# Performance work log

Hardware: AMD Instinct MI355X
Metric: run time of the kernel (lower is better)

Reference implementation:

```python
import jax, jax.numpy as jnp
import numpy as np

D = 4096
H = 4 * D
EPS = 1e-5


def layer_norm(x, g, b):
    mu = jnp.mean(x, axis=-1, keepdims=True)
    var = jnp.mean(jnp.square(x - mu), axis=-1, keepdims=True)
    return (x - mu) * jax.lax.rsqrt(var + EPS) * g + b


def setup_inputs() -> dict:
    key = jax.random.key(0)
    ks = jax.random.split(key, 8)
    s = 0.02
    return {
        "x": jax.random.normal(ks[0], (2, 2048, D), dtype=jnp.float32),
        "Wq": jax.random.normal(ks[1], (D, D), dtype=jnp.float32) * s,
        "bq": jnp.zeros((D,), jnp.float32),
        "Wk": jax.random.normal(ks[2], (D, D), dtype=jnp.float32) * s,
        "bk": jnp.zeros((D,), jnp.float32),
        "Wv": jax.random.normal(ks[3], (D, D), dtype=jnp.float32) * s,
        "bv": jnp.zeros((D,), jnp.float32),
        "Wo": jax.random.normal(ks[4], (D, D), dtype=jnp.float32) * s,
        "bo": jnp.zeros((D,), jnp.float32),
        "g1": jnp.ones((D,), jnp.float32),
        "b1": jnp.zeros((D,), jnp.float32),
        "g2": jnp.ones((D,), jnp.float32),
        "b2": jnp.zeros((D,), jnp.float32),
        "W1": jax.random.normal(ks[5], (D, H), dtype=jnp.float32) * s,
        "bi1": jnp.zeros((H,), jnp.float32),
        "W2": jax.random.normal(ks[6], (H, D), dtype=jnp.float32) * s,
        "bi2": jnp.zeros((D,), jnp.float32),
    }


def reference(x, Wq, bq, Wk, bk, Wv, bv, Wo, bo, g1, b1, g2, b2, W1, bi1, W2, bi2):
    # single-head attention, scale = sqrt(D) (as in the source)
    Q = x @ Wq + bq          # [B, S, D]
    K = x @ Wk + bk
    V = x @ Wv + bv
    scores = jnp.einsum("bsd,btd->bst", Q, K) / jnp.sqrt(jnp.float32(D))
    attn = jax.nn.softmax(scores, axis=-1) @ V   # [B, S, D]
    x = attn @ Wo + bo + x
    x = layer_norm(x, g1, b1)
    h = jax.nn.gelu(x @ W1 + bi1, approximate=False)  # torch nn.GELU default = exact erf
    x = h @ W2 + bi2 + x
    x = layer_norm(x, g2, b2)
    return x
```

## Files before the change

### kernel.cpp

```cpp
#include <hip/hip_runtime.h>
#include <hip/hip_bf16.h>

typedef __bf16 bf16x8 __attribute__((ext_vector_type(8)));
typedef float  f32x4  __attribute__((ext_vector_type(4)));
typedef unsigned short u16;
typedef unsigned int   u32;

#define DEV __device__ __forceinline__

DEV u16 f2bu(float f){ union{float f; u32 i;} x; x.f=f; u32 r=x.i+0x7FFFu+((x.i>>16)&1u); return (u16)(r>>16); }
DEV u32 pack2(float a, float b){ return (u32)f2bu(a) | ((u32)f2bu(b)<<16); }

DEV void gload16(const u16* g, u16* l){
  __builtin_amdgcn_global_load_lds((const __attribute__((address_space(1))) void*)g,
                                   (__attribute__((address_space(3))) void*)l, 16, 0, 0);
}

template<int BIAS, int GELU, int RESF32, int OUTF32>
DEV void gemm_body(
    const u16* __restrict__ A, const u16* __restrict__ Bt,
    const float* __restrict__ bias, const float* __restrict__ resid,
    float* __restrict__ outF, u16* __restrict__ outB,
    int M, int N, int K, int SWZ,
    long long sA, long long sB, long long sC)
{
  __shared__ __align__(16) u16 As[4][8192];
  __shared__ __align__(16) u16 Bs[4][8192];

  const int tid  = threadIdx.x;
  const int lane = tid & 63;
  const int wave = tid >> 6;
  const int wm = wave >> 2;
  const int wn = wave & 3;

  int bx = blockIdx.x, by = blockIdx.y;
  if (SWZ) {
    const int gx = gridDim.x, gy = gridDim.y;
    const int f  = by * gx + bx;
    const int S  = gy << 4;
    const int s  = f / S;
    const int r  = f - s * S;
    bx = (s << 4) + (r & 15);
    by = r >> 4;
  }
  const int rowBase = by * 256;
  const int colBase = bx * 256;

  const u16* Ag = A + (size_t)blockIdx.z * sA + (size_t)rowBase * K;
  const u16* Bg = Bt + (size_t)blockIdx.z * sB + (size_t)colBase * K;

  const int qsw = (lane & 3) ^ ((lane >> 3) & 3);
  const u16* apA0 = Ag + (size_t)(wave*32 + (lane>>2)) * K + qsw*8;
  const u16* apA1 = apA0 + (size_t)16 * K;
  const u16* apB0 = Bg + (size_t)(wave*32 + (lane>>2)) * K + qsw*8;
  const u16* apB1 = apB0 + (size_t)16 * K;
  u16* dA0 = &As[0][wave*1024 + lane*8];
  u16* dA1 = dA0 + 512;
  u16* dB0 = &Bs[0][wave*1024 + lane*8];
  u16* dB1 = dB0 + 512;

#define STAGE(t) { const int _b = (t) & 3; const size_t _k = (size_t)(t) * 32;          \
    gload16(apA0 + _k, dA0 + _b*8192); gload16(apA1 + _k, dA1 + _b*8192);               \
    gload16(apB0 + _k, dB0 + _b*8192); gload16(apB1 + _k, dB1 + _b*8192); }

  const int r15 = lane & 15;
  const int gp  = (lane >> 4) ^ ((lane >> 1) & 3);
  const u16* rdA = &As[0][(wm*128 + r15)*32 + gp*8];
  const u16* rdB = &Bs[0][(wn*64  + r15)*32 + gp*8];

  f32x4 acc[8][4];
  const f32x4 fz = {0.f,0.f,0.f,0.f};
#pragma unroll
  for (int m=0;m<8;++m)
#pragma unroll
    for (int n=0;n<4;++n) acc[m][n] = fz;

  const int KT = K >> 5;
  STAGE(0);
  if (KT > 1) STAGE(1);
  if (KT > 2) STAGE(2);

  for (int t = 0; t < KT; ++t) {
    const int rem = KT - t;
    if (rem > 2)      asm volatile("s_waitcnt vmcnt(8)" ::: "memory");
    else if (rem > 1) asm volatile("s_waitcnt vmcnt(4)" ::: "memory");
    else              asm volatile("s_waitcnt vmcnt(0)" ::: "memory");
    __builtin_amdgcn_s_barrier();
    asm volatile("" ::: "memory");

    const u16* pa = rdA + (t & 3) * 8192;
    const u16* pb = rdB + (t & 3) * 8192;
    bf16x8 a[8], b[4];
#pragma unroll
    for (int m=0;m<8;++m) a[m] = *(const bf16x8*)(pa + m*512);
#pragma unroll
    for (int n=0;n<4;++n) b[n] = *(const bf16x8*)(pb + n*512);

    if (t + 3 < KT) STAGE(t + 3);

    __builtin_amdgcn_s_setprio(1);
#pragma unroll
    for (int m=0;m<8;++m)
#pragma unroll
      for (int n=0;n<4;++n)
        acc[m][n] = __builtin_amdgcn_mfma_f32_16x16x32_bf16(a[m], b[n], acc[m][n], 0,0,0);
    __builtin_amdgcn_s_setprio(0);
  }
#undef STAGE

  const long long cb = (long long)blockIdx.z * sC;
  const int q4 = (lane >> 4) * 4;
#pragma unroll
  for (int m=0;m<8;++m){
    const int row0 = rowBase + wm*128 + m*16 + q4;
#pragma unroll
    for (int n=0;n<4;++n){
      const int col = colBase + wn*64 + n*16 + r15;
      float bb = 0.f;
      if (BIAS) bb = bias[col];
#pragma unroll
      for (int r=0;r<4;++r){
        float v = acc[m][n][r] + bb;
        if (GELU) v = 0.5f*v*(1.f+erff(v*0.70710678118654752f));
        const size_t oi = (size_t)cb + (size_t)(row0+r)*N + col;
        if (RESF32) v += resid[oi];
        if (OUTF32) outF[oi] = v;
        else        outB[oi] = f2bu(v);
      }
    }
  }
}

template<int OUTF32>
DEV void gemm128_body(
    const u16* __restrict__ A, const u16* __restrict__ Bt,
    float* __restrict__ outF, u16* __restrict__ outB,
    int M, int N, int K,
    long long sA, long long sB, long long sC)
{
  __shared__ __align__(16) u16 As[4][4096];
  __shared__ __align__(16) u16 Bs[4][8192];

  const int tid  = threadIdx.x;
  const int lane = tid & 63;
  const int wave = tid >> 6;
  const int wm = wave >> 2;
  const int wn = wave & 3;

  const int rowBase = blockIdx.y * 128;
  const int colBase = blockIdx.x * 256;

  const u16* Ag = A + (size_t)blockIdx.z * sA + (size_t)rowBase * K;
  const u16* Bg = Bt + (size_t)blockIdx.z * sB + (size_t)colBase * K;

  const int qsw = (lane & 3) ^ ((lane >> 3) & 3);
  const u16* apA0 = Ag + (size_t)(wave*16 + (lane>>2)) * K + qsw*8;
  const u16* apB0 = Bg + (size_t)(wave*32 + (lane>>2)) * K + qsw*8;
  const u16* apB1 = apB0 + (size_t)16 * K;
  u16* dA0 = &As[0][wave*512  + lane*8];
  u16* dB0 = &Bs[0][wave*1024 + lane*8];
  u16* dB1 = dB0 + 512;

#define STAGE1(t) { const int _b = (t) & 3; const size_t _k = (size_t)(t) * 32;         \
    gload16(apA0 + _k, dA0 + _b*4096);                                                  \
    gload16(apB0 + _k, dB0 + _b*8192); gload16(apB1 + _k, dB1 + _b*8192); }

  const int r15 = lane & 15;
  const int gp  = (lane >> 4) ^ ((lane >> 1) & 3);
  const u16* rdA = &As[0][(wm*64 + r15)*32 + gp*8];
  const u16* rdB = &Bs[0][(wn*64 + r15)*32 + gp*8];

  f32x4 acc[4][4];
  const f32x4 fz = {0.f,0.f,0.f,0.f};
#pragma unroll
  for (int m=0;m<4;++m)
#pragma unroll
    for (int n=0;n<4;++n) acc[m][n] = fz;

  const int KT = K >> 5;
  STAGE1(0);
  if (KT > 1) STAGE1(1);
  if (KT > 2) STAGE1(2);

  for (int t = 0; t < KT; ++t) {
    const int rem = KT - t;
    if (rem > 2)      asm volatile("s_waitcnt vmcnt(6)" ::: "memory");
    else if (rem > 1) asm volatile("s_waitcnt vmcnt(3)" ::: "memory");
    else              asm volatile("s_waitcnt vmcnt(0)" ::: "memory");
    __builtin_amdgcn_s_barrier();
    asm volatile("" ::: "memory");

    const u16* pa = rdA + (t & 3) * 4096;
    const u16* pb = rdB + (t & 3) * 8192;
    bf16x8 a[4], b[4];
#pragma unroll
    for (int m=0;m<4;++m) a[m] = *(const bf16x8*)(pa + m*512);
#pragma unroll
    for (int n=0;n<4;++n) b[n] = *(const bf16x8*)(pb + n*512);

    if (t + 3 < KT) STAGE1(t + 3);

    __builtin_amdgcn_s_setprio(1);
#pragma unroll
    for (int m=0;m<4;++m)
#pragma unroll
      for (int n=0;n<4;++n)
        acc[m][n] = __builtin_amdgcn_mfma_f32_16x16x32_bf16(a[m], b[n], acc[m][n], 0,0,0);
    __builtin_amdgcn_s_setprio(0);
  }
#undef STAGE1

  const long long cb = (long long)blockIdx.z * sC;
  const int q4 = (lane >> 4) * 4;
#pragma unroll
  for (int m=0;m<4;++m){
    const int row0 = rowBase + wm*64 + m*16 + q4;
#pragma unroll
    for (int n=0;n<4;++n){
      const int col = colBase + wn*64 + n*16 + r15;
#pragma unroll
      for (int r=0;r<4;++r){
        const float v = acc[m][n][r];
        const size_t oi = (size_t)cb + (size_t)(row0+r)*N + col;
        if (OUTF32) outF[oi] = v;
        else        outB[oi] = f2bu(v);
      }
    }
  }
}

#define GEMM_KERNEL(NAME, BIAS, GELU, RESF32, OUTF32)                      \
__global__ __launch_bounds__(512, 2) void NAME(                           \
    const u16* __restrict__ A, const u16* __restrict__ Bt,                 \
    const float* __restrict__ bias, const float* __restrict__ resid,       \
    float* __restrict__ outF, u16* __restrict__ outB,                      \
    int M, int N, int K, int SWZ,                                          \
    long long sA, long long sB, long long sC) {                            \
  gemm_body<BIAS,GELU,RESF32,OUTF32>(A,Bt,bias,resid,outF,outB,M,N,K,SWZ,sA,sB,sC); }

GEMM_KERNEL(gemm_q,   1,0,0,0)
GEMM_KERNEL(gemm_k,   1,0,0,0)
GEMM_KERNEL(gemm_v,   1,0,0,0)
GEMM_KERNEL(gemm_pv,  0,0,0,0)
GEMM_KERNEL(gemm_o,   1,0,1,1)
GEMM_KERNEL(gemm_f1,  1,1,0,0)
GEMM_KERNEL(gemm_f2,  1,0,1,1)

__global__ __launch_bounds__(512, 2) void gemm_qkt(
    const u16* __restrict__ A, const u16* __restrict__ Bt,
    float* __restrict__ outF, u16* __restrict__ outB,
    int M, int N, int K,
    long long sA, long long sB, long long sC) {
  gemm128_body<1>(A, Bt, outF, outB, M, N, K, sA, sB, sC);
}

__global__ __launch_bounds__(256) void tr_f32_bf16(
    const float* __restrict__ in, u16* __restrict__ out, int R, int C)
{
  __shared__ float tile[64][65];
  const int t = threadIdx.x;
  const int tr = blockIdx.y*64, tc = blockIdx.x*64;
  const int c4 = (t&15)*4;
#pragma unroll
  for (int i=0;i<4;++i){
    const int r = i*16 + (t>>4);
    const float4 v = *reinterpret_cast<const float4*>(&in[(size_t)(tr+r)*C + tc + c4]);
    tile[r][c4+0]=v.x; tile[r][c4+1]=v.y; tile[r][c4+2]=v.z; tile[r][c4+3]=v.w;
  }
  __syncthreads();
#pragma unroll
  for (int i=0;i<4;++i){
    const int c = i*16 + (t>>4);
    uint2 o;
    o.x = pack2(tile[c4+0][c], tile[c4+1][c]);
    o.y = pack2(tile[c4+2][c], tile[c4+3][c]);
    *reinterpret_cast<uint2*>(&out[(size_t)(tc+c)*R + tr + c4]) = o;
  }
}

__global__ __launch_bounds__(256) void tr_bf16(
    const u16* __restrict__ in, u16* __restrict__ out, int R, int C,
    long long sIn, long long sOut)
{
  __shared__ u16 tile[64][72];
  const long long z = blockIdx.z;
  in  += z*sIn; out += z*sOut;
  const int t = threadIdx.x;
  const int tr = blockIdx.y*64, tc = blockIdx.x*64;
  const int c4 = (t&15)*4;
#pragma unroll
  for (int i=0;i<4;++i){
    const int r = i*16 + (t>>4);
    const uint2 v = *reinterpret_cast<const uint2*>(&in[(size_t)(tr+r)*C + tc + c4]);
    tile[r][c4+0]=(u16)(v.x&0xffffu); tile[r][c4+1]=(u16)(v.x>>16);
    tile[r][c4+2]=(u16)(v.y&0xffffu); tile[r][c4+3]=(u16)(v.y>>16);
  }
  __syncthreads();
#pragma unroll
  for (int i=0;i<4;++i){
    const int c = i*16 + (t>>4);
    uint2 o;
    o.x = (u32)tile[c4+0][c] | ((u32)tile[c4+1][c]<<16);
    o.y = (u32)tile[c4+2][c] | ((u32)tile[c4+3][c]<<16);
    *reinterpret_cast<uint2*>(&out[(size_t)(tc+c)*R + tr + c4]) = o;
  }
}

__global__ __launch_bounds__(256) void cvt_f32_bf16(
    const float* __restrict__ in, u16* __restrict__ out, int n4)
{
  const int i = blockIdx.x*256 + threadIdx.x;
  if (i >= n4) return;
  const float4 v = reinterpret_cast<const float4*>(in)[i];
  uint2 o; o.x = pack2(v.x,v.y); o.y = pack2(v.z,v.w);
  reinterpret_cast<uint2*>(out)[i] = o;
}

__global__ __launch_bounds__(256) void softmax2048(
    const float* __restrict__ S, u16* __restrict__ P, float scale)
{
  const size_t row = blockIdx.x;
  const float4* src = reinterpret_cast<const float4*>(S + row*2048);
  const int t = threadIdx.x, lane = t&63, wave = t>>6;
  const float4 a = src[t], b = src[t+256];
  float v[8] = {a.x,a.y,a.z,a.w,b.x,b.y,b.z,b.w};
  float m = -3.4e38f;
#pragma unroll
  for (int i=0;i<8;++i){ v[i]*=scale; m = fmaxf(m, v[i]); }
#pragma unroll
  for (int o=32;o>0;o>>=1) m = fmaxf(m, __shfl_xor(m, o));
  __shared__ float red[8];
  if (lane==0) red[wave]=m;
  __syncthreads();
  m = fmaxf(fmaxf(red[0],red[1]), fmaxf(red[2],red[3]));
  float s = 0.f;
#pragma unroll
  for (int i=0;i<8;++i){ v[i] = __expf(v[i]-m); s += v[i]; }
#pragma unroll
  for (int o=32;o>0;o>>=1) s += __shfl_xor(s, o);
  if (lane==0) red[4+wave]=s;
  __syncthreads();
  s = red[4]+red[5]+red[6]+red[7];
  const float r = 1.f/s;
  uint2 o1, o2;
  o1.x = pack2(v[0]*r, v[1]*r); o1.y = pack2(v[2]*r, v[3]*r);
  o2.x = pack2(v[4]*r, v[5]*r); o2.y = pack2(v[6]*r, v[7]*r);
  uint2* dst = reinterpret_cast<uint2*>(P + row*2048);
  dst[t] = o1; dst[t+256] = o2;
}

template<int WB>
__global__ __launch_bounds__(256) void layernorm4096(
    const float* __restrict__ X, const float* __restrict__ g,
    const float* __restrict__ b, float* __restrict__ Yf, u16* __restrict__ Yb)
{
  const size_t row = blockIdx.x;
  const float4* src = reinterpret_cast<const float4*>(X + row*4096);
  const int t = threadIdx.x, lane = t&63, wave = t>>6;
  float4 xv[4];
  float sum=0.f, ss=0.f;
#pragma unroll
  for (int i=0;i<4;++i){
    xv[i] = src[t + 256*i];
    sum += xv[i].x+xv[i].y+xv[i].z+xv[i].w;
    ss  += xv[i].x*xv[i].x + xv[i].y*xv[i].y + xv[i].z*xv[i].z + xv[i].w*xv[i].w;
  }
#pragma unroll
  for (int o=32;o>0;o>>=1){ sum += __shfl_xor(sum,o); ss += __shfl_xor(ss,o); }
  __shared__ float rs[4], rq[4];
  if (lane==0){ rs[wave]=sum; rq[wave]=ss; }
  __syncthreads();
  sum = rs[0]+rs[1]+rs[2]+rs[3];
  ss  = rq[0]+rq[1]+rq[2]+rq[3];
  const float mean = sum * (1.f/4096.f);
  const float var  = ss * (1.f/4096.f) - mean*mean;
  const float rstd = rsqrtf(var + 1e-5f);
#pragma unroll
  for (int i=0;i<4;++i){
    const int i4 = t + 256*i;
    const float4 gv = reinterpret_cast<const float4*>(g)[i4];
    const float4 bvv = reinterpret_cast<const float4*>(b)[i4];
    float4 y;
    y.x = (xv[i].x-mean)*rstd*gv.x + bvv.x;
    y.y = (xv[i].y-mean)*rstd*gv.y + bvv.y;
    y.z = (xv[i].z-mean)*rstd*gv.z + bvv.z;
    y.w = (xv[i].w-mean)*rstd*gv.w + bvv.w;
    reinterpret_cast<float4*>(Yf + row*4096)[i4] = y;
    if (WB){
      uint2 o; o.x = pack2(y.x,y.y); o.y = pack2(y.z,y.w);
      reinterpret_cast<uint2*>(Yb + row*4096)[i4] = o;
    }
  }
}

extern "C" void kernel_launch(void* const* d_in, const int* in_sizes, int n_in,
                              void* d_out, int out_size, void* d_ws, size_t ws_size,
                              hipStream_t stream)
{
  constexpr int D = 4096, HD = 16384, S = 2048, B = 2;
  constexpr int NT = B*S;
  const float* x   = (const float*)d_in[0];
  const float* Wq  = (const float*)d_in[1];
  const float* bq  = (const float*)d_in[2];
  const float* Wk  = (const float*)d_in[3];
  const float* bk  = (const float*)d_in[4];
  const float* Wv  = (const float*)d_in[5];
  const float* bvp = (const float*)d_in[6];
  const float* Wo  = (const float*)d_in[7];
  const float* bo  = (const float*)d_in[8];
  const float* g1  = (const float*)d_in[9];
  const float* b1  = (const float*)d_in[10];
  const float* g2  = (const float*)d_in[11];
  const float* b2  = (const float*)d_in[12];
  const float* W1  = (const float*)d_in[13];
  const float* bi1 = (const float*)d_in[14];
  const float* W2  = (const float*)d_in[15];
  const float* bi2 = (const float*)d_in[16];

  char* ws = (char*)d_ws;
  const size_t MB32 = 33554432;
  u16* WqT = (u16*)(ws + 0*MB32);
  u16* WkT = (u16*)(ws + 1*MB32);
  u16* WvT = (u16*)(ws + 2*MB32);
  u16* WoT = (u16*)(ws + 3*MB32);
  u16* W1T = (u16*)(ws + 0*MB32);
  u16* xb  = (u16*)(ws + 4*MB32);
  u16* Qb  = (u16*)(ws + 5*MB32);
  u16* Kb  = (u16*)(ws + 6*MB32);
  u16* Vb  = (u16*)(ws + 7*MB32);
  u16* W2T = (u16*)(ws + 4*MB32);
  u16* Vt  = (u16*)(ws + 8*MB32);
  float* scoresF = (float*)(ws + 9*MB32);
  u16* Pb  = (u16*)(ws + 10*MB32);
  u16* Ab  = (u16*)(ws + 10*MB32 + 16777216);
  u16* hB  = (u16*)(ws + 8*MB32);
  float* x1raw = (float*)(ws + 12*MB32);
  float* x2raw = (float*)(ws + 12*MB32);
  float* x1f   = (float*)(ws + 14*MB32);
  u16*   x1b   = (u16*)(ws + 16*MB32);

  const dim3 blk(256), blkG(512);
  const long long SD = (long long)S*D, SS = (long long)S*S, DS = (long long)D*S;

  tr_f32_bf16<<<dim3(D/64, D/64), blk, 0, stream>>>(Wq, WqT, D, D);
  tr_f32_bf16<<<dim3(D/64, D/64), blk, 0, stream>>>(Wk, WkT, D, D);
  tr_f32_bf16<<<dim3(D/64, D/64), blk, 0, stream>>>(Wv, WvT, D, D);
  tr_f32_bf16<<<dim3(D/64, D/64), blk, 0, stream>>>(Wo, WoT, D, D);
  cvt_f32_bf16<<<dim3((NT*D/4)/256), blk, 0, stream>>>(x, xb, NT*D/4);

  gemm_q<<<dim3(D/256, NT/256, 1), blkG, 0, stream>>>(xb, WqT, bq,  nullptr, nullptr, Qb, NT, D, D, 1, 0,0,0);
  gemm_k<<<dim3(D/256, NT/256, 1), blkG, 0, stream>>>(xb, WkT, bk,  nullptr, nullptr, Kb, NT, D, D, 1, 0,0,0);
  gemm_v<<<dim3(D/256, NT/256, 1), blkG, 0, stream>>>(xb, WvT, bvp, nullptr, nullptr, Vb, NT, D, D, 1, 0,0,0);
  tr_bf16<<<dim3(D/64, S/64, B), blk, 0, stream>>>(Vb, Vt, S, D, SD, SD);

  gemm_qkt<<<dim3(S/256, S/128, B), blkG, 0, stream>>>(Qb, Kb, scoresF, nullptr, S, S, D, SD, SD, SS);
  softmax2048<<<dim3(B*S), blk, 0, stream>>>(scoresF, Pb, 0.015625f);
  gemm_pv<<<dim3(D/256, S/256, B), blkG, 0, stream>>>(Pb, Vt, nullptr, nullptr, nullptr, Ab, S, D, S, 0, SS, DS, SD);

  gemm_o<<<dim3(D/256, NT/256, 1), blkG, 0, stream>>>(Ab, WoT, bo, x, x1raw, nullptr, NT, D, D, 1, 0,0,0);
  layernorm4096<1><<<dim3(NT), blk, 0, stream>>>(x1raw, g1, b1, x1f, x1b);

  tr_f32_bf16<<<dim3(HD/64, D/64), blk, 0, stream>>>(W1, W1T, D, HD);
  gemm_f1<<<dim3(HD/256, NT/256, 1), blkG, 0, stream>>>(x1b, W1T, bi1, nullptr, nullptr, hB, NT, HD, D, 1, 0,0,0);
  tr_f32_bf16<<<dim3(D/64, HD/64), blk, 0, stream>>>(W2, W2T, HD, D);
  gemm_f2<<<dim3(D/256, NT/256, 1), blkG, 0, stream>>>(hB, W2T, bi2, x1f, x2raw, nullptr, NT, D, HD, 1, 0,0,0);
  layernorm4096<0><<<dim3(NT), blk, 0, stream>>>(x2raw, g2, b2, (float*)d_out, nullptr);
}
```

Measured before the change: 2.183 ms.

## Add 8-wave ping-pong GEMM with K=64 tiles for the two FFN GEMMs

Adds a new GEMM body that uses K=64 tiles with a 2-stage LDS double buffer and an XOR-swizzled layout. Each iteration is split into four MFMA quadrants, and global-to-LDS staging and LDS fragment reads are interleaved between barriers. The two FFN GEMMs, which dominate the FLOPs, are switched to it, while the attention GEMMs stay on the old 4-stage K=32 kernel. It trades a deeper prefetch pipeline for finer-grained overlap, at the cost of many more barriers per iteration.

```diff
diff --git a/kernel.cpp b/kernel.cpp
--- a/kernel.cpp
+++ b/kernel.cpp
@@ -15,6 +15,10 @@
   __builtin_amdgcn_global_load_lds((const __attribute__((address_space(1))) void*)g,
                                    (__attribute__((address_space(3))) void*)l, 16, 0, 0);
 }
+
+#define FENCE asm volatile("" ::: "memory")
+#define BAR   __builtin_amdgcn_s_barrier()
+#define LGKM0 asm volatile("s_waitcnt lgkmcnt(0)" ::: "memory")
 
 template<int BIAS, int GELU, int RESF32, int OUTF32>
 DEV void gemm_body(
@@ -26,12 +30,10 @@
 {
   __shared__ __align__(16) u16 As[4][8192];
   __shared__ __align__(16) u16 Bs[4][8192];
-
   const int tid  = threadIdx.x;
   const int lane = tid & 63;
   const int wave = tid >> 6;
-  const int wm = wave >> 2;
-  const int wn = wave & 3;
+  const int wm = wave >> 2, wn = wave & 3;
 
   int bx = blockIdx.x, by = blockIdx.y;
   if (SWZ) {
@@ -85,8 +87,7 @@
     if (rem > 2)      asm volatile("s_waitcnt vmcnt(8)" ::: "memory");
     else if (rem > 1) asm volatile("s_waitcnt vmcnt(4)" ::: "memory");
     else              asm volatile("s_waitcnt vmcnt(0)" ::: "memory");
-    __builtin_amdgcn_s_barrier();
-    asm volatile("" ::: "memory");
+    BAR; FENCE;
 
     const u16* pa = rdA + (t & 3) * 8192;
     const u16* pb = rdB + (t & 3) * 8192;
@@ -131,6 +132,180 @@
   }
 }
 
+template<int BIAS, int GELU, int RESF32, int OUTF32>
+DEV void gemm8_body(
+    const u16* __restrict__ A, const u16* __restrict__ Bt,
+    const float* __restrict__ bias, const float* __restrict__ resid,
+    float* __restrict__ outF, u16* __restrict__ outB,
+    int M, int N, int K, int SWZ,
+    long long sA, long long sB, long long sC)
+{
+  __shared__ __align__(16) u16 As[2][2][8192];
+  __shared__ __align__(16) u16 Bs[2][2][8192];
+
+  const int tid  = threadIdx.x;
+  const int lane = tid & 63;
+  const int wave = tid >> 6;
+  const int wm = wave >> 2;
+  const int wn = wave & 3;
+
+  int bx = blockIdx.x, by = blockIdx.y;
+  if (SWZ) {
+    const int gx = gridDim.x, gy = gridDim.y;
+    const int f  = by * gx + bx;
+    const int S  = gy << 4;
+    const int s  = f / S;
+    const int r  = f - s * S;
+    bx = (s << 4) + (r & 15);
+    by = r >> 4;
+  }
+  const int rowBase = by * 256;
+  const int colBase = bx * 256;
+
+  const u16* Ag = A + (size_t)blockIdx.z * sA + (size_t)rowBase * K;
+  const u16* Bg = Bt + (size_t)blockIdx.z * sB + (size_t)colBase * K;
+
+  const int swzk = ((tid & 7) ^ ((tid >> 3) & 7)) * 8;
+  const u16* gAh[2], *gBh[2];
+  gAh[0] = Ag + (size_t)(tid>>3) * K + swzk;
+  gAh[1] = Ag + (size_t)(128 + (tid>>3)) * K + swzk;
+  gBh[0] = Bg + (size_t)(tid>>3) * K + swzk;
+  gBh[1] = Bg + (size_t)(128 + (tid>>3)) * K + swzk;
+  const size_t rstep = (size_t)64 * K;
+  u16* dAb = &As[0][0][0] + tid*8;
+  u16* dBb = &Bs[0][0][0] + tid*8;
+
+#define STG_A(h, tt) { u16* _d = dAb + (((tt)&1)<<14) + ((h)<<13);                      \
+    const u16* _g = gAh[h] + (size_t)(tt)*64;                                           \
+    gload16(_g, _d); gload16(_g + rstep, _d + 4096); }
+#define STG_B(h, tt) { u16* _d = dBb + (((tt)&1)<<14) + ((h)<<13);                      \
+    const u16* _g = gBh[h] + (size_t)(tt)*64;                                           \
+    gload16(_g, _d); gload16(_g + rstep, _d + 4096); }
+
+  const int r15 = lane & 15;
+  const int c4 = lane >> 4, e = lane & 7;
+  const int ch0 = (c4 ^ e) * 8;
+  const int ch1 = ((4 + c4) ^ e) * 8;
+  const u16* rA0 = &As[0][wm][0] + r15*64 + ch0;
+  const u16* rA1 = &As[0][wm][0] + r15*64 + ch1;
+  const u16* rB0 = &Bs[0][wn>>1][0] + ((wn&1)*64 + r15)*64 + ch0;
+  const u16* rB1 = &Bs[0][wn>>1][0] + ((wn&1)*64 + r15)*64 + ch1;
+
+  f32x4 acc[8][4];
+  const f32x4 fz = {0.f,0.f,0.f,0.f};
+#pragma unroll
+  for (int m=0;m<8;++m)
+#pragma unroll
+    for (int n=0;n<4;++n) acc[m][n] = fz;
+
+  const int KT = K >> 6;
+  STG_A(0,0); STG_A(1,0); STG_B(0,0); STG_B(1,0);
+  if (KT > 1) {
+    STG_A(0,1); STG_B(0,1); STG_B(1,1);
+    asm volatile("s_waitcnt vmcnt(6)" ::: "memory");
+  } else {
+    asm volatile("s_waitcnt vmcnt(0)" ::: "memory");
+  }
+  BAR; FENCE;
+
+  for (int t = 0; t < KT; ++t) {
+    const int dsel = (t & 1) << 14;
+    const bool s1 = (t + 1 < KT), s2 = (t + 2 < KT);
+    const u16* pa0 = rA0 + dsel; const u16* pa1 = rA1 + dsel;
+    const u16* pb0 = rB0 + dsel; const u16* pb1 = rB1 + dsel;
+    bf16x8 a[4][2], b0[2][2], b1[2][2];
+
+#pragma unroll
+    for (int i=0;i<4;++i){ a[i][0] = *(const bf16x8*)(pa0 + i*1024);
+                           a[i][1] = *(const bf16x8*)(pa1 + i*1024); }
+#pragma unroll
+    for (int n=0;n<2;++n){ b0[n][0] = *(const bf16x8*)(pb0 + n*1024);
+                           b0[n][1] = *(const bf16x8*)(pb1 + n*1024); }
+    if (s1) STG_A(1, t+1);
+    FENCE; BAR; LGKM0;
+    __builtin_amdgcn_s_setprio(1);
+#pragma unroll
+    for (int m=0;m<4;++m)
+#pragma unroll
+      for (int n=0;n<2;++n){
+        acc[m][n] = __builtin_amdgcn_mfma_f32_16x16x32_bf16(a[m][0], b0[n][0], acc[m][n], 0,0,0);
+        acc[m][n] = __builtin_amdgcn_mfma_f32_16x16x32_bf16(a[m][1], b0[n][1], acc[m][n], 0,0,0);
+      }
+    __builtin_amdgcn_s_setprio(0);
+    FENCE; BAR;
+
+#pragma unroll
+    for (int n=0;n<2;++n){ b1[n][0] = *(const bf16x8*)(pb0 + (2+n)*1024);
+                           b1[n][1] = *(const bf16x8*)(pb1 + (2+n)*1024); }
+    FENCE; BAR; LGKM0;
+    __builtin_amdgcn_s_setprio(1);
+#pragma unroll
+    for (int m=0;m<4;++m)
+#pragma unroll
+      for (int n=0;n<2;++n){
+        acc[m][2+n] = __builtin_amdgcn_mfma_f32_16x16x32_bf16(a[m][0], b1[n][0], acc[m][2+n], 0,0,0);
+        acc[m][2+n] = __builtin_amdgcn_mfma_f32_16x16x32_bf16(a[m][1], b1[n][1], acc[m][2+n], 0,0,0);
+      }
+    __builtin_amdgcn_s_setprio(0);
+    FENCE; BAR;
+
+#pragma unroll
+    for (int i=0;i<4;++i){ a[i][0] = *(const bf16x8*)(pa0 + (4+i)*1024);
+                           a[i][1] = *(const bf16x8*)(pa1 + (4+i)*1024); }
+    if (s2) STG_B(0, t+2);
+    FENCE; BAR; LGKM0;
+    __builtin_amdgcn_s_setprio(1);
+#pragma unroll
+    for (int m=0;m<4;++m)
+#pragma unroll
+      for (int n=0;n<2;++n){
+        acc[4+m][2+n] = __builtin_amdgcn_mfma_f32_16x16x32_bf16(a[m][0], b1[n][0], acc[4+m][2+n], 0,0,0);
+        acc[4+m][2+n] = __builtin_amdgcn_mfma_f32_16x16x32_bf16(a[m][1], b1[n][1], acc[4+m][2+n], 0,0,0);
+      }
+    __builtin_amdgcn_s_setprio(0);
+    FENCE; BAR;
+
+    if (s2) { STG_A(0, t+2); STG_B(1, t+2);
+              asm volatile("s_waitcnt vmcnt(6)" ::: "memory"); }
+    else    { asm volatile("s_waitcnt vmcnt(0)" ::: "memory"); }
+    FENCE; BAR;
+    __builtin_amdgcn_s_setprio(1);
+#pragma unroll
+    for (int m=0;m<4;++m)
+#pragma unroll
+      for (int n=0;n<2;++n){
+        acc[4+m][n] = __builtin_amdgcn_mfma_f32_16x16x32_bf16(a[m][0], b0[n][0], acc[4+m][n], 0,0,0);
+        acc[4+m][n] = __builtin_amdgcn_mfma_f32_16x16x32_bf16(a[m][1], b0[n][1], acc[4+m][n], 0,0,0);
+      }
+    __builtin_amdgcn_s_setprio(0);
+    FENCE; BAR;
+  }
+#undef STG_A
+#undef STG_B
+
+  const long long cb = (long long)blockIdx.z * sC;
+  const int q4 = (lane >> 4) * 4;
+#pragma unroll
+  for (int m=0;m<8;++m){
+    const int row0 = rowBase + wm*128 + m*16 + q4;
+#pragma unroll
+    for (int n=0;n<4;++n){
+      const int col = colBase + wn*64 + n*16 + r15;
+      float bb = 0.f;
+      if (BIAS) bb = bias[col];
+#pragma unroll
+      for (int r=0;r<4;++r){
+        float v = acc[m][n][r] + bb;
+        if (GELU) v = 0.5f*v*(1.f+erff(v*0.70710678118654752f));
+        const size_t oi = (size_t)cb + (size_t)(row0+r)*N + col;
+        if (RESF32) v += resid[oi];
+        if (OUTF32) outF[oi] = v;
+        else        outB[oi] = f2bu(v);
+      }
+    }
+  }
+}
+
 template<int OUTF32>
 DEV void gemm128_body(
     const u16* __restrict__ A, const u16* __restrict__ Bt,
@@ -140,12 +315,10 @@
 {
   __shared__ __align__(16) u16 As[4][4096];
   __shared__ __align__(16) u16 Bs[4][8192];
-
   const int tid  = threadIdx.x;
   const int lane = tid & 63;
   const int wave = tid >> 6;
-  const int wm = wave >> 2;
-  const int wn = wave & 3;
+  const int wm = wave >> 2, wn = wave & 3;
 
   const int rowBase = blockIdx.y * 128;
   const int colBase = blockIdx.x * 256;
@@ -187,8 +360,7 @@
     if (rem > 2)      asm volatile("s_waitcnt vmcnt(6)" ::: "memory");
     else if (rem > 1) asm volatile("s_waitcnt vmcnt(3)" ::: "memory");
     else              asm volatile("s_waitcnt vmcnt(0)" ::: "memory");
-    __builtin_amdgcn_s_barrier();
-    asm volatile("" ::: "memory");
+    BAR; FENCE;
 
     const u16* pa = rdA + (t & 3) * 4096;
     const u16* pb = rdB + (t & 3) * 8192;
@@ -229,22 +401,22 @@
   }
 }
 
-#define GEMM_KERNEL(NAME, BIAS, GELU, RESF32, OUTF32)                      \
+#define GEMM_KERNEL(NAME, BODY, BIAS, GELU, RESF32, OUTF32)                \
 __global__ __launch_bounds__(512, 2) void NAME(                           \
     const u16* __restrict__ A, const u16* __restrict__ Bt,                 \
     const float* __restrict__ bias, const float* __restrict__ resid,       \
     float* __restrict__ outF, u16* __restrict__ outB,                      \
     int M, int N, int K, int SWZ,                                          \
     long long sA, long long sB, long long sC) {                            \
-  gemm_body<BIAS,GELU,RESF32,OUTF32>(A,Bt,bias,resid,outF,outB,M,N,K,SWZ,sA,sB,sC); }
-
-GEMM_KERNEL(gemm_q,   1,0,0,0)
-GEMM_KERNEL(gemm_k,   1,0,0,0)
-GEMM_KERNEL(gemm_v,   1,0,0,0)
-GEMM_KERNEL(gemm_pv,  0,0,0,0)
-GEMM_KERNEL(gemm_o,   1,0,1,1)
-GEMM_KERNEL(gemm_f1,  1,1,0,0)
-GEMM_KERNEL(gemm_f2,  1,0,1,1)
+  BODY<BIAS,GELU,RESF32,OUTF32>(A,Bt,bias,resid,outF,outB,M,N,K,SWZ,sA,sB,sC); }
+
+GEMM_KERNEL(gemm_q,   gemm_body,  1,0,0,0)
+GEMM_KERNEL(gemm_k,   gemm_body,  1,0,0,0)
+GEMM_KERNEL(gemm_v,   gemm_body,  1,0,0,0)
+GEMM_KERNEL(gemm_pv,  gemm_body,  0,0,0,0)
+GEMM_KERNEL(gemm_o,   gemm_body,  1,0,1,1)
+GEMM_KERNEL(gemm8_f1, gemm8_body, 1,1,0,0)
+GEMM_KERNEL(gemm8_f2, gemm8_body, 1,0,1,1)
 
 __global__ __launch_bounds__(512, 2) void gemm_qkt(
     const u16* __restrict__ A, const u16* __restrict__ Bt,
@@ -461,8 +633,8 @@
   layernorm4096<1><<<dim3(NT), blk, 0, stream>>>(x1raw, g1, b1, x1f, x1b);
 
   tr_f32_bf16<<<dim3(HD/64, D/64), blk, 0, stream>>>(W1, W1T, D, HD);
-  gemm_f1<<<dim3(HD/256, NT/256, 1), blkG, 0, stream>>>(x1b, W1T, bi1, nullptr, nullptr, hB, NT, HD, D, 1, 0,0,0);
+  gemm8_f1<<<dim3(HD/256, NT/256, 1), blkG, 0, stream>>>(x1b, W1T, bi1, nullptr, nullptr, hB, NT, HD, D, 1, 0,0,0);
   tr_f32_bf16<<<dim3(D/64, HD/64), blk, 0, stream>>>(W2, W2T, HD, D);
-  gemm_f2<<<dim3(D/256, NT/256, 1), blkG, 0, stream>>>(hB, W2T, bi2, x1f, x2raw, nullptr, NT, D, HD, 1, 0,0,0);
+  gemm8_f2<<<dim3(D/256, NT/256, 1), blkG, 0, stream>>>(hB, W2T, bi2, x1f, x2raw, nullptr, NT, D, HD, 1, 0,0,0);
   layernorm4096<0><<<dim3(NT), blk, 0, stream>>>(x2raw, g2, b2, (float*)d_out, nullptr);
 }
```

New measurement: 2.224 ms. About the same (+1.9%).
